# Kernel optimization log

Hardware: AMD Instinct MI355X
Metric: run time of the kernel (lower is better)

Reference implementation:

```python
import jax, jax.numpy as jnp
import numpy as np

N_NODES = 50000
N_EDGES = 800000
N_FEAT = 100
HIDDEN = 100
N_CLASSES = 2
N_GRAPHS = 256


def setup_inputs() -> dict:
    key = jax.random.key(0)
    ks = jax.random.split(key, 16)
    x = jax.random.normal(ks[0], (N_NODES, N_FEAT), dtype=jnp.float32)
    edge_index = jax.random.randint(ks[1], (2, N_EDGES), 0, N_NODES, dtype=jnp.int64)
    batch = jnp.sort(jax.random.randint(ks[2], (N_NODES,), 0, N_GRAPHS, dtype=jnp.int64))
    def lin(k, fan_in, fan_out):
        s = 1.0 / np.sqrt(fan_in)
        return jax.random.uniform(k, (fan_in, fan_out), jnp.float32, -s, s)
    return {
        "x": x, "edge_index": edge_index, "batch": batch,
        # SAGEConv1: lin_l (neighbor aggr, with bias), lin_r (root, no bias)
        "W1l": lin(ks[3], N_FEAT, HIDDEN), "b1": jnp.zeros((HIDDEN,), jnp.float32), "W1r": lin(ks[4], N_FEAT, HIDDEN),
        "W2l": lin(ks[5], HIDDEN, HIDDEN), "b2": jnp.zeros((HIDDEN,), jnp.float32), "W2r": lin(ks[6], HIDDEN, HIDDEN),
        "W3l": lin(ks[7], HIDDEN, HIDDEN), "b3": jnp.zeros((HIDDEN,), jnp.float32), "W3r": lin(ks[8], HIDDEN, HIDDEN),
        "Wlin": lin(ks[9], HIDDEN, N_CLASSES), "blin": jnp.zeros((N_CLASSES,), jnp.float32),
    }


def _sage_conv(x, src, dst, Wl, b, Wr):
    # PyG SAGEConv with mean aggregation: out = lin_l(mean_{j in N(i)} x_j) + lin_r(x_i)
    msg = x[src]  # [E, d] gather
    s = jax.ops.segment_sum(msg, dst, num_segments=x.shape[0])  # [N, d]
    cnt = jax.ops.segment_sum(jnp.ones_like(dst, dtype=x.dtype), dst, num_segments=x.shape[0])
    aggr = s / jnp.maximum(cnt, 1.0)[:, None]
    return aggr @ Wl + b + x @ Wr


def reference(x, edge_index, batch, W1l, b1, W1r, W2l, b2, W2r, W3l, b3, W3r, Wlin, blin):
    src, dst = edge_index[0], edge_index[1]
    h = jax.nn.relu(_sage_conv(x, src, dst, W1l, b1, W1r))
    h = jax.nn.relu(_sage_conv(h, src, dst, W2l, b2, W2r))
    h = _sage_conv(h, src, dst, W3l, b3, W3r)
    # global_mean_pool over batch ids
    gs = jax.ops.segment_sum(h, batch, num_segments=N_GRAPHS)
    gc = jax.ops.segment_sum(jnp.ones_like(batch, dtype=h.dtype), batch, num_segments=N_GRAPHS)
    g = gs / jnp.maximum(gc, 1.0)[:, None]
    # dropout(p=0.5) is identity in eval mode
    return g @ Wlin + blin
```

## Files before the change

### kernel.cpp

```cpp
#include <hip/hip_runtime.h>
#include <hip/hip_bf16.h>

typedef __attribute__((ext_vector_type(8))) short short8v;
typedef __attribute__((ext_vector_type(4))) float f32x4;

#define PST 128
#define PSTL 136
#define MAXBUCK 1024
#define BCAP 8192

static __device__ inline unsigned short f2bf(float x) {
    union { float f; unsigned int u; } c; c.f = x;
    unsigned int r = (c.u + 0x7FFFu + ((c.u >> 16) & 1u)) >> 16;
    return (unsigned short)r;
}
static __device__ inline float bf2f(unsigned short h) {
    union { float f; unsigned int u; } c; c.u = ((unsigned int)h) << 16;
    return c.f;
}
static __device__ inline f32x4 MF(short8v a, short8v b, f32x4 c) {
    return __builtin_amdgcn_mfma_f32_16x16x32_bf16(a, b, c, 0, 0, 0);
}
static __device__ inline void acc8(float (&a)[8], short8v v) {
#pragma unroll
    for (int m = 0; m < 8; ++m) a[m] += bf2f((unsigned short)v[m]);
}

__global__ __launch_bounds__(256) void k_binscatter(const int* __restrict__ src,
                                                    const int* __restrict__ dst,
                                                    int* __restrict__ bcur,
                                                    int* __restrict__ tmpv,
                                                    int n, int nbuck, int chunk) {
    __shared__ int lcnt[MAXBUCK];
    __shared__ int lbase[MAXBUCK];
    int t = threadIdx.x;
    for (int b = t; b < nbuck; b += 256) lcnt[b] = 0;
    __syncthreads();
    int e0 = blockIdx.x * chunk;
    int e1 = e0 + chunk; if (e1 > n) e1 = n;
    for (int e = e0 + t; e < e1; e += 256) atomicAdd(&lcnt[dst[e] >> 8], 1);
    __syncthreads();
    for (int b = t; b < nbuck; b += 256) {
        int c = lcnt[b];
        lbase[b] = c ? atomicAdd(&bcur[b], c) : 0;
        lcnt[b] = 0;
    }
    __syncthreads();
    for (int e = e0 + t; e < e1; e += 256) {
        int d = dst[e];
        int b = d >> 8;
        int r = atomicAdd(&lcnt[b], 1);
        tmpv[(size_t)b * BCAP + lbase[b] + r] = (src[e] << 8) | (d & 255);
    }
}

__global__ __launch_bounds__(1024) void k_binscan(const int* __restrict__ bcur,
                                                  int* __restrict__ bbase,
                                                  int* __restrict__ rowp,
                                                  int nbuck, int n_nodes, int n_edges) {
    __shared__ int tmp[1024];
    int t = threadIdx.x;
    int v = (t < nbuck) ? bcur[t] : 0;
    tmp[t] = v;
    __syncthreads();
    for (int off = 1; off < 1024; off <<= 1) {
        int u = 0;
        if (t >= off) u = tmp[t - off];
        __syncthreads();
        if (t >= off) tmp[t] += u;
        __syncthreads();
    }
    if (t < nbuck) bbase[t] = tmp[t] - v;
    if (t == 0) rowp[n_nodes] = n_edges;
}

__global__ __launch_bounds__(256) void k_build(const int* __restrict__ tmpv,
                                               const int* __restrict__ bbase,
                                               const int* __restrict__ bcur,
                                               int* __restrict__ rowp,
                                               float* __restrict__ inv,
                                               int* __restrict__ ssrc,
                                               int n_nodes, int nbuck) {
    __shared__ int hist[256];
    __shared__ int scan[256];
    __shared__ int curs[256];
    int b = blockIdx.x;
    int t = threadIdx.x;
    int s = bbase[b];
    int cnt = bcur[b];
    const int* tv = tmpv + (size_t)b * BCAP;
    hist[t] = 0;
    __syncthreads();
    for (int i = t; i < cnt; i += 256) atomicAdd(&hist[tv[i] & 255], 1);
    __syncthreads();
    int v = hist[t];
    scan[t] = v;
    __syncthreads();
    for (int off = 1; off < 256; off <<= 1) {
        int u = 0;
        if (t >= off) u = scan[t - off];
        __syncthreads();
        if (t >= off) scan[t] += u;
        __syncthreads();
    }
    int excl = scan[t] - v;
    curs[t] = excl;
    int node = (b << 8) + t;
    if (node < n_nodes) {
        rowp[node] = s + excl;
        inv[node] = 1.0f / (float)(v > 1 ? v : 1);
    }
    __syncthreads();
    for (int i = t; i < cnt; i += 256) {
        int p = tv[i];
        int r = atomicAdd(&curs[p & 255], 1);
        ssrc[s + r] = p >> 8;
    }
}

__global__ __launch_bounds__(256) void k_cvt(const float* __restrict__ X,
                                             unsigned short* __restrict__ Xhi,
                                             unsigned short* __restrict__ Xlo,
                                             int n) {
    int grp = threadIdx.x >> 4, l = threadIdx.x & 15;
    int i = blockIdx.x * 16 + grp;
    if (i >= n) return;
    unsigned short* ph = Xhi + (size_t)i * PST + l * 8;
    unsigned short* pl = Xlo + (size_t)i * PST + l * 8;
    if (l < 13) {
        float4 v0 = *(const float4*)(X + (size_t)i * 100 + l * 8);
        float4 v1 = (l < 12) ? *(const float4*)(X + (size_t)i * 100 + l * 8 + 4)
                             : make_float4(0.f, 0.f, 0.f, 0.f);
        float f[8] = {v0.x, v0.y, v0.z, v0.w, v1.x, v1.y, v1.z, v1.w};
        short8v hv, lv;
#pragma unroll
        for (int m = 0; m < 8; ++m) {
            unsigned short h = f2bf(f[m]);
            hv[m] = (short)h;
            lv[m] = (short)f2bf(f[m] - bf2f(h));
        }
        *(short8v*)ph = hv;
        *(short8v*)pl = lv;
    } else {
        short8v z = (short8v){0,0,0,0,0,0,0,0};
        *(short8v*)ph = z;
        *(short8v*)pl = z;
    }
}

#define PACKN (2 * 4 * 7 * 64)
__global__ __launch_bounds__(256) void k_pack3(const float* __restrict__ W1l, const float* __restrict__ W1r,
                                               const float* __restrict__ W2l, const float* __restrict__ W2r,
                                               const float* __restrict__ W3l, const float* __restrict__ W3r,
                                               unsigned short* __restrict__ B1h, unsigned short* __restrict__ B1l,
                                               unsigned short* __restrict__ B2h, unsigned short* __restrict__ B2l,
                                               unsigned short* __restrict__ B3h, unsigned short* __restrict__ B3l) {
    int gid = blockIdx.x * 256 + threadIdx.x;
    if (gid >= 3 * PACKN) return;
    int layer = gid / PACKN;
    int idx = gid - layer * PACKN;
    const float* Wl = layer == 0 ? W1l : (layer == 1 ? W2l : W3l);
    const float* Wr = layer == 0 ? W1r : (layer == 1 ? W2r : W3r);
    unsigned short* Bh = layer == 0 ? B1h : (layer == 1 ? B2h : B3h);
    unsigned short* Bl = layer == 0 ? B1l : (layer == 1 ? B2l : B3l);
    int lane = idx & 63;
    int t = idx >> 6;
    int nt = t % 7;
    int pc = t / 7;
    int part = pc >> 2, c = pc & 3;
    int col = nt * 16 + (lane & 15);
    int fbase = c * 32 + (lane >> 4) * 8;
    const float* W = part ? Wr : Wl;
    for (int jj = 0; jj < 8; ++jj) {
        int k = fbase + jj;
        float w = (k < 100 && col < 100) ? W[k * 100 + col] : 0.f;
        unsigned short h = f2bf(w);
        Bh[(size_t)idx * 8 + jj] = h;
        Bl[(size_t)idx * 8 + jj] = f2bf(w - bf2f(h));
    }
}

__global__ __launch_bounds__(128) void k_layer(const unsigned short* __restrict__ Xhi,
                                               const unsigned short* __restrict__ Xlo,
                                               const int* __restrict__ ssrc,
                                               const int* __restrict__ rowp,
                                               const float* __restrict__ inv,
                                               const unsigned short* __restrict__ Bh,
                                               const unsigned short* __restrict__ Bl,
                                               const float* __restrict__ bias,
                                               unsigned short* __restrict__ Ohi,
                                               unsigned short* __restrict__ Olo,
                                               int relu, int n) {
    __shared__ unsigned short lds_h[32][PSTL];
    __shared__ unsigned short lds_l[32][PSTL];
    const int t = threadIdx.x;
    const int wv = t >> 6;
    const int lane = t & 63;
    const int base = blockIdx.x * 32;

    {
        const int grp = lane >> 4, l = lane & 15;
        const bool act = l < 13;
        const size_t loff = (size_t)l * 8;
        const short8v z = (short8v){0,0,0,0,0,0,0,0};
#pragma unroll
        for (int it = 0; it < 4; ++it) {
            const int lr = wv * 16 + it * 4 + grp;
            const int node = base + lr;
            if (node < n) {
                const int s = rowp[node];
                const int e = rowp[node + 1];
                float a[8];
#pragma unroll
                for (int m = 0; m < 8; ++m) a[m] = 0.f;

                int i = s;
                int j0 = 0, j1 = 0, j2 = 0, j3 = 0, j4 = 0, j5 = 0, j6 = 0, j7 = 0;
                if (i + 8 <= e) {
                    j0 = ssrc[i];     j1 = ssrc[i + 1];
                    j2 = ssrc[i + 2]; j3 = ssrc[i + 3];
                    j4 = ssrc[i + 4]; j5 = ssrc[i + 5];
                    j6 = ssrc[i + 6]; j7 = ssrc[i + 7];
                }
                while (i + 8 <= e) {
                    const int ni = i + 8;
                    int k0 = 0, k1 = 0, k2 = 0, k3 = 0, k4 = 0, k5 = 0, k6 = 0, k7 = 0;
                    if (ni + 8 <= e) {
                        k0 = ssrc[ni];     k1 = ssrc[ni + 1];
                        k2 = ssrc[ni + 2]; k3 = ssrc[ni + 3];
                        k4 = ssrc[ni + 4]; k5 = ssrc[ni + 5];
                        k6 = ssrc[ni + 6]; k7 = ssrc[ni + 7];
                    }
                    if (act) {
                        short8v v0 = *(const short8v*)(Xhi + (size_t)j0 * PST + loff);
                        short8v v1 = *(const short8v*)(Xhi + (size_t)j1 * PST + loff);
                        short8v v2 = *(const short8v*)(Xhi + (size_t)j2 * PST + loff);
                        short8v v3 = *(const short8v*)(Xhi + (size_t)j3 * PST + loff);
                        short8v v4 = *(const short8v*)(Xhi + (size_t)j4 * PST + loff);
                        short8v v5 = *(const short8v*)(Xhi + (size_t)j5 * PST + loff);
                        short8v v6 = *(const short8v*)(Xhi + (size_t)j6 * PST + loff);
                        short8v v7 = *(const short8v*)(Xhi + (size_t)j7 * PST + loff);
                        acc8(a, v0); acc8(a, v1); acc8(a, v2); acc8(a, v3);
                        acc8(a, v4); acc8(a, v5); acc8(a, v6); acc8(a, v7);
                    }
                    j0 = k0; j1 = k1; j2 = k2; j3 = k3;
                    j4 = k4; j5 = k5; j6 = k6; j7 = k7;
                    i = ni;
                }
                if (i + 4 <= e) {
                    int s0 = ssrc[i], s1 = ssrc[i + 1], s2 = ssrc[i + 2], s3 = ssrc[i + 3];
                    if (act) {
                        short8v v0 = *(const short8v*)(Xhi + (size_t)s0 * PST + loff);
                        short8v v1 = *(const short8v*)(Xhi + (size_t)s1 * PST + loff);
                        short8v v2 = *(const short8v*)(Xhi + (size_t)s2 * PST + loff);
                        short8v v3 = *(const short8v*)(Xhi + (size_t)s3 * PST + loff);
                        acc8(a, v0); acc8(a, v1); acc8(a, v2); acc8(a, v3);
                    }
                    i += 4;
                }
                for (; i < e; ++i) {
                    int s0 = ssrc[i];
                    if (act) {
                        short8v v0 = *(const short8v*)(Xhi + (size_t)s0 * PST + loff);
                        acc8(a, v0);
                    }
                }

                if (act) {
                    const float f = inv[node];
                    short8v hv, lv;
#pragma unroll
                    for (int m = 0; m < 8; ++m) {
                        float v = a[m] * f;
                        unsigned short h = f2bf(v);
                        hv[m] = (short)h;
                        lv[m] = (short)f2bf(v - bf2f(h));
                    }
                    *(short8v*)&lds_h[lr][l * 8] = hv;
                    *(short8v*)&lds_l[lr][l * 8] = lv;
                } else {
                    *(short8v*)&lds_h[lr][l * 8] = z;
                    *(short8v*)&lds_l[lr][l * 8] = z;
                }
            } else {
                *(short8v*)&lds_h[lr][l * 8] = z;
                *(short8v*)&lds_l[lr][l * 8] = z;
            }
        }
    }
    __builtin_amdgcn_wave_barrier();

    const int m0 = base + wv * 16;
    const int lrow = lane & 15;
    const int lg = lane >> 4;
    const int ldr = wv * 16 + lrow;

    f32x4 acc[7];
#pragma unroll
    for (int nt = 0; nt < 7; ++nt) acc[nt] = (f32x4){0.f, 0.f, 0.f, 0.f};

    int r0 = m0 + lrow; if (r0 >= n) r0 = n - 1;
    const size_t b0 = (size_t)r0 * PST + lg * 8;

#pragma unroll
    for (int c = 0; c < 4; ++c) {
        short8v ah0 = *(const short8v*)&lds_h[ldr][c * 32 + lg * 8];
        short8v al0 = *(const short8v*)&lds_l[ldr][c * 32 + lg * 8];
        const unsigned short* bph = Bh + ((size_t)(c * 7) * 64 + lane) * 8;
        const unsigned short* bpl = Bl + ((size_t)(c * 7) * 64 + lane) * 8;
#pragma unroll
        for (int nt = 0; nt < 7; ++nt) {
            short8v bh = *(const short8v*)(bph + nt * 512);
            short8v bl = *(const short8v*)(bpl + nt * 512);
            acc[nt] = MF(ah0, bh, acc[nt]);
            acc[nt] = MF(ah0, bl, acc[nt]);
            acc[nt] = MF(al0, bh, acc[nt]);
        }
    }
#pragma unroll
    for (int c = 0; c < 4; ++c) {
        short8v ah0 = *(const short8v*)(Xhi + b0 + c * 32);
        short8v al0 = *(const short8v*)(Xlo + b0 + c * 32);
        const unsigned short* bph = Bh + ((size_t)((4 + c) * 7) * 64 + lane) * 8;
        const unsigned short* bpl = Bl + ((size_t)((4 + c) * 7) * 64 + lane) * 8;
#pragma unroll
        for (int nt = 0; nt < 7; ++nt) {
            short8v bh = *(const short8v*)(bph + nt * 512);
            short8v bl = *(const short8v*)(bpl + nt * 512);
            acc[nt] = MF(ah0, bh, acc[nt]);
            acc[nt] = MF(ah0, bl, acc[nt]);
            acc[nt] = MF(al0, bh, acc[nt]);
        }
    }

#pragma unroll
    for (int nt = 0; nt < 7; ++nt) {
        int col = nt * 16 + lrow;
        bool cok = col < 100;
        float bb = cok ? bias[col] : 0.f;
#pragma unroll
        for (int r = 0; r < 4; ++r) {
            int row = m0 + lg * 4 + r;
            if (cok && row < n) {
                float v = acc[nt][r] + bb;
                if (relu) v = fmaxf(v, 0.f);
                unsigned short h = f2bf(v);
                size_t o = (size_t)row * PST + col;
                Ohi[o] = h;
                Olo[o] = f2bf(v - bf2f(h));
            }
        }
    }
    if (lane < 32) {
        int row = m0 + (lane >> 1);
        if (row < n) {
            unsigned short* op = ((lane & 1) == 0 ? Ohi : Olo) + (size_t)row * PST;
            short4 z4 = {0, 0, 0, 0};
            short8v z = (short8v){0,0,0,0,0,0,0,0};
            *(short4*)(op + 100) = z4;
            *(short8v*)(op + 104) = z;
            *(short8v*)(op + 112) = z;
            *(short8v*)(op + 120) = z;
        }
    }
}

__global__ __launch_bounds__(256) void k_pool(const unsigned short* __restrict__ Hhi,
                                              const unsigned short* __restrict__ Hlo,
                                              const int* __restrict__ batch,
                                              const float* __restrict__ Wlin,
                                              const float* __restrict__ blin,
                                              float* __restrict__ out, int n) {
    int g = blockIdx.x;
    int t = threadIdx.x;
    int grp = t >> 4, l = t & 15;
    int lo = 0, hi = n;
    while (lo < hi) { int m = (lo + hi) >> 1; if (batch[m] < g) lo = m + 1; else hi = m; }
    int lo2 = lo, hi2 = n;
    while (lo2 < hi2) { int m = (lo2 + hi2) >> 1; if (batch[m] < g + 1) lo2 = m + 1; else hi2 = m; }

    const bool act = l < 13;
    float a[8];
#pragma unroll
    for (int m = 0; m < 8; ++m) a[m] = 0.f;
    const size_t loff = (size_t)l * 8;
    for (int node = lo + grp; node < lo2; node += 16) {
        if (act) {
            short8v vh = *(const short8v*)(Hhi + (size_t)node * PST + loff);
            short8v vl = *(const short8v*)(Hlo + (size_t)node * PST + loff);
#pragma unroll
            for (int m = 0; m < 8; ++m)
                a[m] += bf2f((unsigned short)vh[m]) + bf2f((unsigned short)vl[m]);
        }
    }

    __shared__ float part[16][13][8];
    if (act) {
#pragma unroll
        for (int m = 0; m < 8; ++m) part[grp][l][m] = a[m];
    }
    __syncthreads();

    __shared__ float gm[104];
    if (t < 104) {
        int fg = t >> 3, m = t & 7;
        float s = 0.f;
#pragma unroll
        for (int q = 0; q < 16; ++q) s += part[q][fg][m];
        float f = (lo2 > lo) ? 1.0f / (float)(lo2 - lo) : 0.0f;
        gm[t] = s * f;
    }
    __syncthreads();
    if (t < 2) {
        float o = blin[t];
        for (int k = 0; k < 100; ++k) o += gm[k] * Wlin[k * 2 + t];
        out[g * 2 + t] = o;
    }
}


extern "C" void kernel_launch(void* const* d_in, const int* in_sizes, int n_in,
                              void* d_out, int out_size, void* d_ws, size_t ws_size,
                              hipStream_t stream) {
    const float* x    = (const float*)d_in[0];
    const int*   ei   = (const int*)d_in[1];
    const int*   batch= (const int*)d_in[2];
    const float* W1l  = (const float*)d_in[3];
    const float* b1   = (const float*)d_in[4];
    const float* W1r  = (const float*)d_in[5];
    const float* W2l  = (const float*)d_in[6];
    const float* b2   = (const float*)d_in[7];
    const float* W2r  = (const float*)d_in[8];
    const float* W3l  = (const float*)d_in[9];
    const float* b3   = (const float*)d_in[10];
    const float* W3r  = (const float*)d_in[11];
    const float* Wlin = (const float*)d_in[12];
    const float* blin = (const float*)d_in[13];
    float* out = (float*)d_out;

    const int n_nodes  = in_sizes[0] / 100;
    const int n_edges  = in_sizes[1] / 2;
    const int n_graphs = out_size / 2;
    const int* src = ei;
    const int* dst = ei + n_edges;

    char* ws = (char*)d_ws;
    size_t o = 0;
    auto alloc = [&](size_t bytes) { size_t r = o; o = (o + bytes + 255) & ~(size_t)255; return r; };
    const int nbuck = (n_nodes + 255) >> 8;
    int*   rowp = (int*)(ws + alloc((size_t)(n_nodes + 1) * 4));
    float* inv  = (float*)(ws + alloc((size_t)n_nodes * 4));
    int*   ssrc = (int*)(ws + alloc((size_t)n_edges * 4));
    int*   bbase= (int*)(ws + alloc(MAXBUCK * 4));
    int*   bcur = (int*)(ws + alloc(MAXBUCK * 4));
    int*   tmpv = (int*)(ws + alloc((size_t)nbuck * BCAP * 4));
    const size_t pbytes = (size_t)n_nodes * PST * 2;
    unsigned short* XAhi = (unsigned short*)(ws + alloc(pbytes));
    unsigned short* XAlo = (unsigned short*)(ws + alloc(pbytes));
    unsigned short* XBhi = (unsigned short*)(ws + alloc(pbytes));
    unsigned short* XBlo = (unsigned short*)(ws + alloc(pbytes));
    const size_t bfb = (size_t)PACKN * 8 * 2;
    unsigned short* B1h = (unsigned short*)(ws + alloc(bfb));
    unsigned short* B1l = (unsigned short*)(ws + alloc(bfb));
    unsigned short* B2h = (unsigned short*)(ws + alloc(bfb));
    unsigned short* B2l = (unsigned short*)(ws + alloc(bfb));
    unsigned short* B3h = (unsigned short*)(ws + alloc(bfb));
    unsigned short* B3l = (unsigned short*)(ws + alloc(bfb));

    hipMemsetAsync(bcur, 0, MAXBUCK * 4, stream);

    const int chunk = (n_edges + 255) / 256;

    k_binscatter<<<256, 256, 0, stream>>>(src, dst, bcur, tmpv, n_edges, nbuck, chunk);
    k_binscan<<<1, 1024, 0, stream>>>(bcur, bbase, rowp, nbuck, n_nodes, n_edges);
    k_build<<<nbuck, 256, 0, stream>>>(tmpv, bbase, bcur, rowp, inv, ssrc,
                                       n_nodes, nbuck);

    k_pack3<<<(3 * PACKN + 255) / 256, 256, 0, stream>>>(
        W1l, W1r, W2l, W2r, W3l, W3r, B1h, B1l, B2h, B2l, B3h, B3l);

    const int nb16 = (n_nodes + 15) / 16;
    const int lgrid = (n_nodes + 31) / 32;

    k_cvt<<<nb16, 256, 0, stream>>>(x, XAhi, XAlo, n_nodes);

    k_layer<<<lgrid, 128, 0, stream>>>(XAhi, XAlo, ssrc, rowp, inv, B1h, B1l, b1,
                                       XBhi, XBlo, 1, n_nodes);
    k_layer<<<lgrid, 128, 0, stream>>>(XBhi, XBlo, ssrc, rowp, inv, B2h, B2l, b2,
                                       XAhi, XAlo, 1, n_nodes);
    k_layer<<<lgrid, 128, 0, stream>>>(XAhi, XAlo, ssrc, rowp, inv, B3h, B3l, b3,
                                       XBhi, XBlo, 0, n_nodes);

    k_pool<<<n_graphs, 256, 0, stream>>>(XBhi, XBlo, batch, Wlin, blin, out, n_nodes);
}
```

Baseline: 221.1 us.

## Sort nodes by in-degree within buckets to balance aggregation work across lanes

The build kernel now computes, per 256-node bucket, a permutation that orders nodes by (clamped) in-degree, with -1 marking padding slots. The layer kernel processes nodes in permuted order, so the 16-lane groups of a wave and the nodes of a 32-node tile have similar degrees. This reduces divergence and idle lanes in the gather loop. In exchange it adds a perm lookup per row and scatters output rows to non-contiguous addresses.

```diff
diff --git a/kernel.cpp b/kernel.cpp
--- a/kernel.cpp
+++ b/kernel.cpp
@@ -80,10 +80,12 @@
                                                int* __restrict__ rowp,
                                                float* __restrict__ inv,
                                                int* __restrict__ ssrc,
+                                               int* __restrict__ perm,
                                                int n_nodes, int nbuck) {
     __shared__ int hist[256];
     __shared__ int scan[256];
     __shared__ int curs[256];
+    __shared__ int dcur[64];
     int b = blockIdx.x;
     int t = threadIdx.x;
     int s = bbase[b];
@@ -106,15 +108,31 @@
     int excl = scan[t] - v;
     curs[t] = excl;
     int node = (b << 8) + t;
-    if (node < n_nodes) {
+    const bool valid = (node < n_nodes);
+    if (valid) {
         rowp[node] = s + excl;
         inv[node] = 1.0f / (float)(v > 1 ? v : 1);
     }
+    perm[node] = -1;
     __syncthreads();
     for (int i = t; i < cnt; i += 256) {
         int p = tv[i];
         int r = atomicAdd(&curs[p & 255], 1);
         ssrc[s + r] = p >> 8;
+    }
+    if (t < 64) dcur[t] = 0;
+    __syncthreads();
+    int dcl = v > 63 ? 63 : v;
+    if (valid) atomicAdd(&dcur[dcl], 1);
+    __syncthreads();
+    if (t == 0) {
+        int c = 0;
+        for (int q = 0; q < 64; ++q) { int h = dcur[q]; dcur[q] = c; c += h; }
+    }
+    __syncthreads();
+    if (valid) {
+        int rank = atomicAdd(&dcur[dcl], 1);
+        perm[(b << 8) + rank] = node;
     }
 }
 
@@ -185,6 +203,7 @@
                                                const int* __restrict__ ssrc,
                                                const int* __restrict__ rowp,
                                                const float* __restrict__ inv,
+                                               const int* __restrict__ perm,
                                                const unsigned short* __restrict__ Bh,
                                                const unsigned short* __restrict__ Bl,
                                                const float* __restrict__ bias,
@@ -206,10 +225,10 @@
 #pragma unroll
         for (int it = 0; it < 4; ++it) {
             const int lr = wv * 16 + it * 4 + grp;
-            const int node = base + lr;
-            if (node < n) {
-                const int s = rowp[node];
-                const int e = rowp[node + 1];
+            const int pn = perm[base + lr];
+            if (pn >= 0) {
+                const int s = rowp[pn];
+                const int e = rowp[pn + 1];
                 float a[8];
 #pragma unroll
                 for (int m = 0; m < 8; ++m) a[m] = 0.f;
@@ -267,7 +286,7 @@
                 }
 
                 if (act) {
-                    const float f = inv[node];
+                    const float f = inv[pn];
                     short8v hv, lv;
 #pragma unroll
                     for (int m = 0; m < 8; ++m) {
@@ -299,7 +318,8 @@
 #pragma unroll
     for (int nt = 0; nt < 7; ++nt) acc[nt] = (f32x4){0.f, 0.f, 0.f, 0.f};
 
-    int r0 = m0 + lrow; if (r0 >= n) r0 = n - 1;
+    const int pn0 = perm[m0 + lrow];
+    const int r0 = pn0 < 0 ? 0 : pn0;
     const size_t b0 = (size_t)r0 * PST + lg * 8;
 
 #pragma unroll
@@ -333,6 +353,9 @@
         }
     }
 
+    int pr[4];
+#pragma unroll
+    for (int r = 0; r < 4; ++r) pr[r] = perm[m0 + lg * 4 + r];
 #pragma unroll
     for (int nt = 0; nt < 7; ++nt) {
         int col = nt * 16 + lrow;
@@ -340,21 +363,20 @@
         float bb = cok ? bias[col] : 0.f;
 #pragma unroll
         for (int r = 0; r < 4; ++r) {
-            int row = m0 + lg * 4 + r;
-            if (cok && row < n) {
+            if (cok && pr[r] >= 0) {
                 float v = acc[nt][r] + bb;
                 if (relu) v = fmaxf(v, 0.f);
                 unsigned short h = f2bf(v);
-                size_t o = (size_t)row * PST + col;
+                size_t o = (size_t)pr[r] * PST + col;
                 Ohi[o] = h;
                 Olo[o] = f2bf(v - bf2f(h));
             }
         }
     }
     if (lane < 32) {
-        int row = m0 + (lane >> 1);
-        if (row < n) {
-            unsigned short* op = ((lane & 1) == 0 ? Ohi : Olo) + (size_t)row * PST;
+        int prow = perm[m0 + (lane >> 1)];
+        if (prow >= 0) {
+            unsigned short* op = ((lane & 1) == 0 ? Ohi : Olo) + (size_t)prow * PST;
             short4 z4 = {0, 0, 0, 0};
             short8v z = (short8v){0,0,0,0,0,0,0,0};
             *(short4*)(op + 100) = z4;
@@ -451,6 +473,7 @@
     int*   rowp = (int*)(ws + alloc((size_t)(n_nodes + 1) * 4));
     float* inv  = (float*)(ws + alloc((size_t)n_nodes * 4));
     int*   ssrc = (int*)(ws + alloc((size_t)n_edges * 4));
+    int*   perm = (int*)(ws + alloc((size_t)nbuck * 256 * 4));
     int*   bbase= (int*)(ws + alloc(MAXBUCK * 4));
     int*   bcur = (int*)(ws + alloc(MAXBUCK * 4));
     int*   tmpv = (int*)(ws + alloc((size_t)nbuck * BCAP * 4));
@@ -473,7 +496,7 @@
 
     k_binscatter<<<256, 256, 0, stream>>>(src, dst, bcur, tmpv, n_edges, nbuck, chunk);
     k_binscan<<<1, 1024, 0, stream>>>(bcur, bbase, rowp, nbuck, n_nodes, n_edges);
-    k_build<<<nbuck, 256, 0, stream>>>(tmpv, bbase, bcur, rowp, inv, ssrc,
+    k_build<<<nbuck, 256, 0, stream>>>(tmpv, bbase, bcur, rowp, inv, ssrc, perm,
                                        n_nodes, nbuck);
 
     k_pack3<<<(3 * PACKN + 255) / 256, 256, 0, stream>>>(
@@ -484,11 +507,11 @@
 
     k_cvt<<<nb16, 256, 0, stream>>>(x, XAhi, XAlo, n_nodes);
 
-    k_layer<<<lgrid, 128, 0, stream>>>(XAhi, XAlo, ssrc, rowp, inv, B1h, B1l, b1,
+    k_layer<<<lgrid, 128, 0, stream>>>(XAhi, XAlo, ssrc, rowp, inv, perm, B1h, B1l, b1,
                                        XBhi, XBlo, 1, n_nodes);
-    k_layer<<<lgrid, 128, 0, stream>>>(XBhi, XBlo, ssrc, rowp, inv, B2h, B2l, b2,
+    k_layer<<<lgrid, 128, 0, stream>>>(XBhi, XBlo, ssrc, rowp, inv, perm, B2h, B2l, b2,
                                        XAhi, XAlo, 1, n_nodes);
-    k_layer<<<lgrid, 128, 0, stream>>>(XAhi, XAlo, ssrc, rowp, inv, B3h, B3l, b3,
+    k_layer<<<lgrid, 128, 0, stream>>>(XAhi, XAlo, ssrc, rowp, inv, perm, B3h, B3l, b3,
                                        XBhi, XBlo, 0, n_nodes);
 
     k_pool<<<n_graphs, 256, 0, stream>>>(XBhi, XBlo, batch, Wlin, blin, out, n_nodes);
```

Result: slower. 233.9 us (+5.8%).
